# Optimization experiments

Hardware: AMD Instinct MI355X
Metric: run time of the kernel (lower is better)

## Reference

```python
import jax, jax.numpy as jnp
import numpy as np

EPS = 1e-5
K_NBR = 21   # num_neighbors + 1 (self)
PSI = 4


def _bn(x, g, b):
    # BatchNorm (training-mode forward): channel-last, normalize over all other axes
    axes = tuple(range(x.ndim - 1))
    m = jnp.mean(x, axis=axes, keepdims=True)
    v = jnp.var(x, axis=axes, keepdims=True)
    return (x - m) * jax.lax.rsqrt(v + EPS) * g + b


def setup_inputs() -> dict:
    key = jax.random.key(0)
    ks = jax.random.split(key, 16)
    B, N, Cin, Cout = 4, 2048, 64, 256
    h = Cout // 2
    w_ch = Cout // PSI
    heads = 2 * PSI - 1

    def w(k, o, i):
        return jax.random.normal(k, (o, i), dtype=jnp.float32) * (1.0 / np.sqrt(i))

    p = {}
    p['xyz'] = jax.random.normal(ks[0], (B, N, 3), dtype=jnp.float32)
    p['f'] = jax.random.normal(ks[1], (B, Cin, N), dtype=jnp.float32)
    p['W_geo'] = w(ks[2], h, 6);       p['g_geo'] = jnp.ones(h);   p['b_geo'] = jnp.zeros(h)
    p['W_feat'] = w(ks[3], h, 2 * Cin); p['g_feat'] = jnp.ones(h); p['b_feat'] = jnp.zeros(h)
    p['g_bn'] = jnp.ones(Cout); p['b_bn'] = jnp.zeros(Cout)
    p['W_q'] = w(ks[4], Cout, Cout); p['g_q'] = jnp.ones(Cout); p['b_q'] = jnp.zeros(Cout)
    p['W_k'] = w(ks[5], Cout, Cout); p['g_k'] = jnp.ones(Cout); p['b_k'] = jnp.zeros(Cout)
    p['W_v'] = w(ks[6], Cout, Cout); p['g_v'] = jnp.ones(Cout); p['b_v'] = jnp.zeros(Cout)
    p['W_fus'] = w(ks[7], Cout, heads * w_ch); p['bias_fus'] = jnp.zeros(Cout)
    p['g_fus'] = jnp.ones(Cout); p['b_fus'] = jnp.zeros(Cout)
    p['g_ln'] = jnp.ones(Cout); p['b_ln'] = jnp.zeros(Cout)
    p['W_mlp'] = w(ks[8], Cout, Cout); p['bias_mlp'] = jnp.zeros(Cout)
    return p


def reference(xyz, f, W_geo, g_geo, b_geo, W_feat, g_feat, b_feat, g_bn, b_bn,
              W_q, g_q, b_q, W_k, g_k, b_k, W_v, g_v, b_v,
              W_fus, bias_fus, g_fus, b_fus, g_ln, b_ln, W_mlp, bias_mlp):
    B, N, _ = xyz.shape
    Cout = g_bn.shape[0]
    w_ch = Cout // PSI
    d_sh = w_ch // 2
    heads = 2 * PSI - 1

    # ---- PositionFusion: KNN grouping ----
    sq = jnp.sum(xyz * xyz, axis=-1)                                   # [B,N]
    d2 = sq[:, :, None] + sq[:, None, :] - 2.0 * jnp.einsum('bnd,bmd->bnm', xyz, xyz)
    _, idx = jax.lax.top_k(-d2, K_NBR)                                 # [B,N,K]

    grouped_xyz = jax.vmap(lambda p, i: p[i])(xyz, idx)                # [B,N,K,3]
    xyz_diff = grouped_xyz - xyz[:, :, None, :]
    geo_in = jnp.concatenate(
        [jnp.broadcast_to(xyz[:, :, None, :], grouped_xyz.shape), xyz_diff], axis=-1)  # [B,N,K,6]

    ft = jnp.transpose(f, (0, 2, 1))                                   # [B,N,Cin]
    grouped_f = jax.vmap(lambda p, i: p[i])(ft, idx)                   # [B,N,K,Cin]
    feat_in = jnp.concatenate(
        [grouped_f, jnp.broadcast_to(ft[:, :, None, :], grouped_f.shape)], axis=-1)    # [B,N,K,2Cin]

    geo = jax.nn.relu(_bn(jnp.einsum('bnki,oi->bnko', geo_in, W_geo), g_geo, b_geo))
    fea = jax.nn.relu(_bn(jnp.einsum('bnki,oi->bnko', feat_in, W_feat), g_feat, b_feat))
    feature_ = jnp.max(jnp.concatenate([geo, fea], axis=-1), axis=2)   # [B,N,Cout] (maxpool over K)

    # ---- BatchNorm1d ----
    x = _bn(feature_, g_bn, b_bn)

    # ---- Shifted-channel multi-head attention ----
    q = jax.nn.relu(_bn(jnp.einsum('bnc,oc->bno', x, W_q), g_q, b_q))
    k = jax.nn.relu(_bn(jnp.einsum('bnc,oc->bno', x, W_k), g_k, b_k))
    v = jax.nn.relu(_bn(jnp.einsum('bnc,oc->bno', x, W_v), g_v, b_v))

    qh = jnp.stack([q[..., m * d_sh:m * d_sh + w_ch] for m in range(heads)], axis=1)  # [B,H,N,w]
    kh = jnp.stack([k[..., m * d_sh:m * d_sh + w_ch] for m in range(heads)], axis=1)
    vh = jnp.stack([v[..., m * d_sh:m * d_sh + w_ch] for m in range(heads)], axis=1)

    a = jax.nn.softmax(jnp.einsum('bhnc,bhmc->bhnm', qh, kh), axis=-1)  # [B,H,N,N]
    o = jnp.einsum('bhnm,bhmc->bhnc', a, vh)                            # [B,H,N,w]
    O = jnp.transpose(o, (0, 2, 1, 3)).reshape(B, N, heads * w_ch)      # channel-concat per head

    fus = jax.nn.relu(_bn(jnp.einsum('bnc,oc->bno', O, W_fus) + bias_fus, g_fus, b_fus))

    feature__ = fus + feature_                                          # residual

    # ---- LayerNorm over channels ----
    m = jnp.mean(feature__, axis=-1, keepdims=True)
    var = jnp.var(feature__, axis=-1, keepdims=True)
    y = (feature__ - m) * jax.lax.rsqrt(var + EPS) * g_ln + b_ln

    out = feature__ + (jnp.einsum('bnc,oc->bno', y, W_mlp) + bias_mlp)
    return jnp.transpose(out, (0, 2, 1))                                # [B,Cout,N] like torch
```

## Files before the change

### kernel.cpp

```cpp
#include <hip/hip_runtime.h>
#include <math.h>

#define NB    4
#define NPTS  2048
#define ROWS  (NB*NPTS)
#define CIN   64
#define COUT  256
#define KNBR  21
#define NHEADS 7
#define WCH   64
#define DSH   32
#define LOG2E 1.4426950408889634f

typedef __attribute__((ext_vector_type(8))) short short8;
typedef __attribute__((ext_vector_type(4))) float floatx4;

#if __has_builtin(__builtin_amdgcn_exp2f)
#define EXP2(x) __builtin_amdgcn_exp2f(x)
#else
#define EXP2(x) __expf((x)*0.6931471805599453f)
#endif
#if __has_builtin(__builtin_amdgcn_rcpf)
#define RCP(x) __builtin_amdgcn_rcpf(x)
#else
#define RCP(x) (1.0f/(x))
#endif

__device__ __forceinline__ ushort f2bf(float x) {
    unsigned u = __float_as_uint(x);
    u += 0x7fffu + ((u >> 16) & 1u);
    return (ushort)(u >> 16);
}

__device__ __forceinline__ unsigned cvt_pk_bf16(float lo, float hi) {
    unsigned r;
    asm("v_cvt_pk_bf16_f32 %0, %1, %2" : "=v"(r) : "v"(lo), "v"(hi));
    return r;
}

template<int CTRL, int RMASK>
__device__ __forceinline__ unsigned dpp_umin_step(unsigned x) {
    unsigned t = (unsigned)__builtin_amdgcn_update_dpp((int)x, (int)x, CTRL, RMASK, 0xF, false);
    return (t < x) ? t : x;
}
__device__ __forceinline__ unsigned wave_min_u32(unsigned x) {
    x = dpp_umin_step<0x111, 0xF>(x);
    x = dpp_umin_step<0x112, 0xF>(x);
    x = dpp_umin_step<0x114, 0xF>(x);
    x = dpp_umin_step<0x118, 0xF>(x);
    x = dpp_umin_step<0x142, 0xA>(x);
    x = dpp_umin_step<0x143, 0xC>(x);
    return (unsigned)__builtin_amdgcn_readlane((int)x, 63);
}

__device__ __forceinline__ unsigned umin2(unsigned a, unsigned b) { return a < b ? a : b; }
__device__ __forceinline__ unsigned umax2(unsigned a, unsigned b) { return a < b ? b : a; }

__device__ __forceinline__ void ins6(unsigned &m1, unsigned &m2, unsigned &m3,
                                     unsigned &m4, unsigned &m5, unsigned &m6, unsigned k) {
    unsigned c = k, t;
    t = umin2(m1, c); c = umax2(m1, c); m1 = t;
    t = umin2(m2, c); c = umax2(m2, c); m2 = t;
    t = umin2(m3, c); c = umax2(m3, c); m3 = t;
    t = umin2(m4, c); c = umax2(m4, c); m4 = t;
    t = umin2(m5, c); c = umax2(m5, c); m5 = t;
    m6 = umin2(m6, c);
}

__global__ __launch_bounds__(256) void prep_knn(const float* __restrict__ f, const float* __restrict__ Wf,
                                                const float* __restrict__ xyz, const float* __restrict__ Wg,
                                                const float* __restrict__ W_q, const float* __restrict__ W_k,
                                                const float* __restrict__ W_v, const float* __restrict__ W_fus,
                                                float* __restrict__ X, float* __restrict__ A,
                                                ushort* __restrict__ Wb, float* __restrict__ sums,
                                                int* __restrict__ idx) {
    __shared__ float4 SXQ[2048];
    int t = threadIdx.x;
    int blk = blockIdx.x;
    if (blk < 512) {
        float* As = (float*)SXQ;
        float* Ws = As + 16*68;
        int bx = blk & 127, by = blk >> 7;
        if (by == 0 && bx < 12) sums[bx*256 + t] = 0.f;
        int gid = (by*128 + bx)*256 + t;
        for (int i = gid; i < 311296; i += 131072) {
            const float* Wsrc; int off;
            if (i < 65536)       { Wsrc = W_q;   off = i; }
            else if (i < 131072) { Wsrc = W_k;   off = i - 65536; }
            else if (i < 196608) { Wsrc = W_v;   off = i - 131072; }
            else                 { Wsrc = W_fus; off = i - 196608; }
            Wb[i] = f2bf(Wsrc[off]);
        }
        int r0 = bx * 64, n0 = by * 64;
        for (int e = t; e < 4096; e += 256) {
            int row = r0 + (e >> 6), c = n0 + (e & 63), cc = c & 127;
            float x = xyz[row*3], y = xyz[row*3+1], z = xyz[row*3+2];
            const float* w = Wg + cc*6;
            float s = (c < 128) ? ((w[3]*x + w[4]*y) + w[5]*z)
                                : (((w[0]-w[3])*x + (w[1]-w[4])*y) + (w[2]-w[5])*z);
            A[(size_t)row*256 + c] = s;
        }
        int b = r0 >> 11, nbase = r0 & 2047;
        int tx = t & 15, ty = t >> 4;
        float acc[4][4];
#pragma unroll
        for (int i = 0; i < 4; i++)
#pragma unroll
            for (int j = 0; j < 4; j++) acc[i][j] = 0.f;
        int m64 = t & 63, kg = t >> 6;
        int lk = t & 15, lm = t >> 4;
        for (int k0 = 0; k0 < 64; k0 += 16) {
#pragma unroll
            for (int p = 0; p < 4; p++) {
                int k = kg*4 + p;
                As[k*68 + m64] = f[(size_t)b*CIN*NPTS + (size_t)(k0 + k)*NPTS + nbase + m64];
            }
#pragma unroll
            for (int i2 = 0; i2 < 4; i2++) {
                int cg = n0 + lm + 16*i2;
                Ws[lk*68 + lm + 16*i2] = Wf[(size_t)(cg & 127)*128 + (cg >> 7)*64 + k0 + lk];
            }
            __syncthreads();
#pragma unroll
            for (int kq = 0; kq < 16; kq++) {
                float4 a  = *(const float4*)&As[kq*68 + 4*ty];
                float4 b4 = *(const float4*)&Ws[kq*68 + 4*tx];
                float av[4] = {a.x, a.y, a.z, a.w};
                float bv[4] = {b4.x, b4.y, b4.z, b4.w};
#pragma unroll
                for (int i = 0; i < 4; i++)
#pragma unroll
                    for (int j = 0; j < 4; j++) acc[i][j] = fmaf(av[i], bv[j], acc[i][j]);
            }
            __syncthreads();
        }
#pragma unroll
        for (int i = 0; i < 4; i++)
#pragma unroll
            for (int j = 0; j < 4; j++)
                X[(size_t)(r0 + 4*ty + i)*256 + n0 + 4*tx + j] = acc[i][j];
        return;
    }
    int kb = blk - 512;
    int b = kb >> 9;
    int g = kb & 511;
    for (int m = t; m < NPTS; m += 256) {
        float x = xyz[(size_t)b*NPTS*3 + m*3];
        float y = xyz[(size_t)b*NPTS*3 + m*3 + 1];
        float z = xyz[(size_t)b*NPTS*3 + m*3 + 2];
        SXQ[m] = make_float4(x, y, z, (x*x + y*y) + z*z);
    }
    __syncthreads();
    int w = t >> 6, lane = t & 63;
    int n = g*4 + w;
    float4 q4 = SXQ[n];
    float qx = q4.x, qy = q4.y, qz = q4.z, sqn = q4.w;

    unsigned key[32];
    unsigned a1 = 0xFFFFFFFFu, a2 = 0xFFFFFFFFu, a3 = 0xFFFFFFFFu,
             a4 = 0xFFFFFFFFu, a5 = 0xFFFFFFFFu, a6 = 0xFFFFFFFFu;
    unsigned c1 = 0xFFFFFFFFu, c2 = 0xFFFFFFFFu, c3 = 0xFFFFFFFFu,
             c4 = 0xFFFFFFFFu, c5 = 0xFFFFFFFFu, c6 = 0xFFFFFFFFu;
#pragma unroll
    for (int i = 0; i < 16; i++) {
        int m = lane + (i << 6);
        float4 p = SXQ[m];
        float dt = (qx*p.x + qy*p.y) + qz*p.z;
        float d2 = fmaxf((sqn + p.w) - 2.0f*dt, 0.f);
        unsigned kv = (__float_as_uint(d2) & 0xFFFFF800u) | (unsigned)m;
        key[i] = kv;
        ins6(a1, a2, a3, a4, a5, a6, kv);
    }
#pragma unroll
    for (int i = 16; i < 32; i++) {
        int m = lane + (i << 6);
        float4 p = SXQ[m];
        float dt = (qx*p.x + qy*p.y) + qz*p.z;
        float d2 = fmaxf((sqn + p.w) - 2.0f*dt, 0.f);
        unsigned kv = (__float_as_uint(d2) & 0xFFFFF800u) | (unsigned)m;
        key[i] = kv;
        ins6(c1, c2, c3, c4, c5, c6, kv);
    }
    ins6(a1, a2, a3, a4, a5, a6, c1);
    ins6(a1, a2, a3, a4, a5, a6, c2);
    ins6(a1, a2, a3, a4, a5, a6, c3);
    ins6(a1, a2, a3, a4, a5, a6, c4);
    ins6(a1, a2, a3, a4, a5, a6, c5);
    ins6(a1, a2, a3, a4, a5, a6, c6);

    unsigned winkey = 0xFFFFFFFFu;
    {
        unsigned fr = a1, p2 = a2, p3 = a3, p4 = a4, p5 = a5, p6 = a6;
#pragma unroll
        for (int kk = 0; kk < 32; kk++) {
            unsigned win = wave_min_u32(fr);
            if (lane == kk) winkey = win;
            bool own = (fr == win);
            fr = own ? p2 : fr;
            p2 = own ? p3 : p2;
            p3 = own ? p4 : p3;
            p4 = own ? p5 : p4;
            p5 = own ? p6 : p5;
            p6 = own ? 0xFFFFFFFFu : p6;
        }
        if (__ballot(fr == 0xFFFFFFFFu) != 0ULL) {
            winkey = 0xFFFFFFFFu;
            for (int kk = 0; kk < 32; kk++) {
                unsigned lv = key[0];
#pragma unroll
                for (int i = 1; i < 32; i++) lv = (key[i] < lv) ? key[i] : lv;
                unsigned win = wave_min_u32(lv);
                if (lane == kk) winkey = win;
                unsigned widx = win & 2047u;
                int slot = (int)(widx >> 6);
                bool own = (lane == (int)(widx & 63u));
#pragma unroll
                for (int i = 0; i < 32; i++)
                    if (i == slot && own) key[i] = 0xFFFFFFFFu;
            }
        }
    }
    double d2r;
    int mr;
    {
        double qx64 = (double)qx, qy64 = (double)qy, qz64 = (double)qz;
        double sqn64 = qx64*qx64 + qy64*qy64 + qz64*qz64;
        if (lane < 32) {
            mr = (int)(winkey & 2047u);
            float4 p = SXQ[mr];
            double x = (double)p.x, y = (double)p.y, z = (double)p.z;
            double sqm = x*x + y*y + z*z;
            double dt  = qx64*x + qy64*y + qz64*z;
            d2r = (sqn64 + sqm) - 2.0*dt;
        } else {
            d2r = INFINITY; mr = 0x7FFFFFFF;
        }
    }
#pragma unroll
    for (int k = 2; k <= 32; k <<= 1) {
#pragma unroll
        for (int j = k >> 1; j > 0; j >>= 1) {
            double od = __shfl_xor(d2r, j, 64);
            int    om = __shfl_xor(mr, j, 64);
            bool up    = ((lane & k) == 0);
            bool lower = ((lane & j) == 0);
            bool oless = (od < d2r) || (od == d2r && om < mr);
            bool keepOther = up ? (lower ? oless : !oless) : (lower ? !oless : oless);
            if (keepOther) { d2r = od; mr = om; }
        }
    }
    if (lane < KNBR)
        idx[((size_t)b*NPTS + n)*KNBR + lane] = mr;
}

__global__ __launch_bounds__(256) void stats_gf(const float* __restrict__ geoBC, const float* __restrict__ featAC,
                                                const int* __restrict__ idx, const float* __restrict__ g_geo,
                                                const float* __restrict__ g_feat,
                                                float* __restrict__ sums, float* __restrict__ xsel) {
    int c = threadIdx.x;
    int cc = c & 127;
    const float* base = (c < 128) ? geoBC : featAC;
    bool wantmax = ((c < 128) ? g_geo[cc] : g_feat[cc]) >= 0.f;
    float s = 0.f, ss = 0.f;
    int r0 = blockIdx.x * 32;
    for (int r = r0; r < r0 + 32; r++) {
        int b = r >> 11;
        float ctr = base[(size_t)r*256 + 128 + cc];
        float mx = -1e30f, mn = 1e30f;
        const int* ip = idx + (size_t)r*KNBR;
        for (int kk = 0; kk < KNBR; kk++) {
            int j = ip[kk];
            float xv = ctr + base[((size_t)(b*NPTS + j))*256 + cc];
            mx = fmaxf(mx, xv); mn = fminf(mn, xv);
            s += xv; ss += xv*xv;
        }
        xsel[(size_t)r*256 + c] = wantmax ? mx : mn;
    }
    atomicAdd(&sums[c], s);
    atomicAdd(&sums[256 + c], ss);
}

__global__ __launch_bounds__(256) void feature_maxsel(const float* __restrict__ xsel, const float* __restrict__ sums,
                                                      const float* __restrict__ g_geo, const float* __restrict__ b_geo,
                                                      const float* __restrict__ g_feat, const float* __restrict__ b_feat,
                                                      float* __restrict__ feat, float* __restrict__ sums_bn1) {
    int c = threadIdx.x;
    const float inv = 1.0f / (float)(ROWS*KNBR);
    float mean = sums[c]*inv;
    float var  = sums[256+c]*inv - mean*mean;
    float g  = (c < 128) ? g_geo[c] : g_feat[c-128];
    float bb = (c < 128) ? b_geo[c] : b_feat[c-128];
    float sc = g / sqrtf(var + 1e-5f);
    float tt = bb - mean*sc;
    float s = 0.f, ss = 0.f;
    int r0 = blockIdx.x*32;
    for (int r = r0; r < r0+32; r++) {
        size_t i = (size_t)r*256 + c;
        float y = fmaxf(fmaf(sc, xsel[i], tt), 0.f);
        feat[i] = y; s += y; ss += y*y;
    }
    atomicAdd(&sums_bn1[c], s); atomicAdd(&sums_bn1[256+c], ss);
}

__global__ __launch_bounds__(256) void gemm_qkv(const float* __restrict__ Af, const float* __restrict__ sums_in,
                                                const float* __restrict__ g_bn, const float* __restrict__ b_bn,
                                                const ushort* __restrict__ Wb,
                                                float* __restrict__ QKVF, float* __restrict__ sums) {
    __shared__ float bns[2][256];
    __shared__ float red[4][256][2];
    int t = threadIdx.x;
    int r0 = blockIdx.x * 64, g = blockIdx.y;
    int w = t >> 6, lane = t & 63;
    int r15 = lane & 15, quad = lane >> 4;
    {
        float mean = sums_in[512 + t] * (1.0f/(float)ROWS);
        float var  = sums_in[768 + t] * (1.0f/(float)ROWS) - mean*mean;
        float sc = g_bn[t] / sqrtf(var + 1e-5f);
        bns[0][t] = sc;
        bns[1][t] = b_bn[t] - mean*sc;
    }
    __syncthreads();
    short8 aq[8];
    {
        const float* ap = Af + (size_t)(r0 + 16*w + r15)*256;
#pragma unroll
        for (int kc = 0; kc < 8; kc++) {
            int k0 = 32*kc + 8*quad;
            float4 a0 = *(const float4*)&ap[k0];
            float4 a1 = *(const float4*)&ap[k0+4];
            float4 s0 = *(const float4*)&bns[0][k0];
            float4 s1 = *(const float4*)&bns[0][k0+4];
            float4 h0 = *(const float4*)&bns[1][k0];
            float4 h1 = *(const float4*)&bns[1][k0+4];
            ushort u8[8];
            u8[0] = f2bf(fmaf(s0.x, a0.x, h0.x)); u8[1] = f2bf(fmaf(s0.y, a0.y, h0.y));
            u8[2] = f2bf(fmaf(s0.z, a0.z, h0.z)); u8[3] = f2bf(fmaf(s0.w, a0.w, h0.w));
            u8[4] = f2bf(fmaf(s1.x, a1.x, h1.x)); u8[5] = f2bf(fmaf(s1.y, a1.y, h1.y));
            u8[6] = f2bf(fmaf(s1.z, a1.z, h1.z)); u8[7] = f2bf(fmaf(s1.w, a1.w, h1.w));
            aq[kc] = *(short8*)u8;
        }
    }
    floatx4 zero4 = {0.f, 0.f, 0.f, 0.f};
    floatx4 acc[16];
#pragma unroll
    for (int st = 0; st < 16; st++) acc[st] = zero4;
    const ushort* wbase = Wb + (size_t)g*65536 + (size_t)r15*256 + 8*quad;
#pragma unroll
    for (int st = 0; st < 16; st++) {
        const ushort* wp = wbase + (size_t)(16*st)*256;
#pragma unroll
        for (int kc = 0; kc < 8; kc++) {
            short8 bf = *(const short8*)(wp + 32*kc);
            acc[st] = __builtin_amdgcn_mfma_f32_16x16x32_bf16(aq[kc], bf, acc[st], 0, 0, 0);
        }
    }
#pragma unroll
    for (int st = 0; st < 16; st++) {
        float s  = (acc[st][0] + acc[st][1]) + (acc[st][2] + acc[st][3]);
        float q2 = (acc[st][0]*acc[st][0] + acc[st][1]*acc[st][1]) +
                   (acc[st][2]*acc[st][2] + acc[st][3]*acc[st][3]);
        s  += __shfl_xor(s, 16, 64);  s  += __shfl_xor(s, 32, 64);
        q2 += __shfl_xor(q2, 16, 64); q2 += __shfl_xor(q2, 32, 64);
        if (lane < 16) { red[w][16*st + r15][0] = s; red[w][16*st + r15][1] = q2; }
#pragma unroll
        for (int reg = 0; reg < 4; reg++)
            QKVF[(size_t)(r0 + 16*w + 4*quad + reg)*768 + g*256 + 16*st + r15] = acc[st][reg];
    }
    __syncthreads();
    {
        float s = red[0][t][0] + red[1][t][0] + red[2][t][0] + red[3][t][0];
        float q = red[0][t][1] + red[1][t][1] + red[2][t][1] + red[3][t][1];
        atomicAdd(&sums[1024 + g*512 + t], s);
        atomicAdd(&sums[1024 + g*512 + 256 + t], q);
    }
}

__global__ __launch_bounds__(256) void affine_qkv(const float* __restrict__ QKVF, const float* __restrict__ sums,
                                                  const float* __restrict__ g_q, const float* __restrict__ b_q,
                                                  const float* __restrict__ g_k, const float* __restrict__ b_k,
                                                  const float* __restrict__ g_v, const float* __restrict__ b_v,
                                                  ushort* __restrict__ qk, ushort* __restrict__ vt) {
    __shared__ float sts[6][256];
    __shared__ ushort tile[64][72];
    int t = threadIdx.x;
    {
        const float* gs[3] = {g_q, g_k, g_v};
        const float* bs[3] = {b_q, b_k, b_v};
#pragma unroll
        for (int g = 0; g < 3; g++) {
            float mean = sums[1024 + g*512 + t] * (1.0f/(float)ROWS);
            float var  = sums[1024 + g*512 + 256 + t] * (1.0f/(float)ROWS) - mean*mean;
            float sc = gs[g][t] / sqrtf(var + 1e-5f);
            float sh = bs[g][t] - mean*sc;
            if (g == 0) { sc *= LOG2E; sh *= LOG2E; }
            sts[2*g][t] = sc;
            sts[2*g+1][t] = sh;
        }
    }
    __syncthreads();
    int r0 = blockIdx.x * 64, c0 = blockIdx.y * 64;
    int b = r0 >> 11, nbase = r0 & 2047;
    if (c0 < 512) {
#pragma unroll
        for (int rep = 0; rep < 16; rep++) {
            int e = t + 256*rep;
            int row = e >> 6, c = e & 63;
            int col = c0 + c, g = col >> 8, cc = col & 255;
            float v = QKVF[(size_t)(r0 + row)*768 + col];
            v = fmaxf(fmaf(sts[2*g][cc], v, sts[2*g+1][cc]), 0.f);
            qk[(size_t)(r0 + row)*512 + col] = f2bf(v);
        }
    } else {
#pragma unroll
        for (int rep = 0; rep < 16; rep++) {
            int e = t + 256*rep;
            int row = e >> 6, c = e & 63;
            int col = c0 + c, cc = col & 255;
            float v = QKVF[(size_t)(r0 + row)*768 + col];
            v = fmaxf(fmaf(sts[4][cc], v, sts[5][cc]), 0.f);
            tile[c][row] = f2bf(v);
        }
        __syncthreads();
#pragma unroll
        for (int rep = 0; rep < 16; rep++) {
            int e = t + 256*rep;
            int cc = e >> 6, nn = e & 63;
            vt[((size_t)(b*256 + (c0 - 512) + cc))*2048 + nbase + nn] = tile[cc][nn];
        }
    }
}

__global__ __launch_bounds__(512) void attn2(const ushort* __restrict__ qk, const ushort* __restrict__ vt,
                                             float* __restrict__ obuf) {
    __shared__ ushort Ksh[2][64*72];
    __shared__ ushort Vts[2][64*72];
    __shared__ ushort Psh[128*72];
    int h = blockIdx.y, b = blockIdx.z;
    int r0 = blockIdx.x * 128;
    int t = threadIdx.x;
    int w = t >> 6, lane = t & 63;
    int r15 = lane & 15, quad = lane >> 4;
    size_t rowbase = (size_t)b*NPTS;
    int hoff = h*DSH;
    int rr = t >> 3, c8 = t & 7;

    const ushort* ksrc = qk + (rowbase + rr)*512 + 256 + hoff + 8*c8;
    const ushort* vsrc = vt + ((size_t)(b*256 + hoff + rr))*2048 + 8*c8;
    int ldst = rr*72 + 8*c8;

    short8 aq[2];
#pragma unroll
    for (int s = 0; s < 2; s++)
        aq[s] = *(const short8*)(qk + (rowbase + r0 + 16*w + r15)*512 + hoff + 32*s + 8*quad);

    {
        uint4 k0 = *(const uint4*)(ksrc);
        uint4 v0 = *(const uint4*)(vsrc);
        *(uint4*)&Ksh[0][ldst] = k0;
        *(uint4*)&Vts[0][ldst] = v0;
    }

    floatx4 zero4 = {0.f, 0.f, 0.f, 0.f};
    floatx4 oacc[4];
    float mrun = -1e30f, lrun = 0.f;
#pragma unroll
    for (int i = 0; i < 4; i++) oacc[i] = zero4;

    ushort* prow = &Psh[(16*w + r15)*72];

    asm volatile("s_waitcnt lgkmcnt(0)" ::: "memory");
    __builtin_amdgcn_s_barrier();
    __builtin_amdgcn_sched_barrier(0);

    int cur = 0;
    for (int m0 = 0; m0 < NPTS; m0 += 64) {
        int mnext = (m0 + 64 < NPTS) ? (m0 + 64) : 0;
        uint4 kreg = *(const uint4*)(ksrc + (size_t)mnext*512);
        uint4 vreg = *(const uint4*)(vsrc + mnext);

        const ushort* Kc = Ksh[cur];
        const ushort* Vc = Vts[cur];

        floatx4 sacc[4];
#pragma unroll
        for (int tt = 0; tt < 4; tt++) sacc[tt] = zero4;
        __builtin_amdgcn_s_setprio(1);
#pragma unroll
        for (int tt = 0; tt < 4; tt++) {
            int key = 16*tt + r15;
#pragma unroll
            for (int s = 0; s < 2; s++) {
                short8 kf = *(const short8*)&Kc[key*72 + 32*s + 8*quad];
                sacc[tt] = __builtin_amdgcn_mfma_f32_16x16x32_bf16(kf, aq[s], sacc[tt], 0, 0, 0);
            }
        }
        __builtin_amdgcn_s_setprio(0);

        float mx = sacc[0][0];
#pragma unroll
        for (int tt = 0; tt < 4; tt++)
#pragma unroll
            for (int reg = 0; reg < 4; reg++) mx = fmaxf(mx, sacc[tt][reg]);
        mx = fmaxf(mx, __shfl_xor(mx, 16, 64));
        mx = fmaxf(mx, __shfl_xor(mx, 32, 64));

        if (!__all(mx <= mrun)) {
            float mnew = fmaxf(mrun, mx);
            float alpha = EXP2(mrun - mnew);
            lrun *= alpha;
#pragma unroll
            for (int td = 0; td < 4; td++) oacc[td] *= alpha;
            mrun = mnew;
        }

        float rs = 0.f;
#pragma unroll
        for (int tt = 0; tt < 4; tt++) {
            float p0 = EXP2(sacc[tt][0] - mrun);
            float p1 = EXP2(sacc[tt][1] - mrun);
            float p2 = EXP2(sacc[tt][2] - mrun);
            float p3 = EXP2(sacc[tt][3] - mrun);
            rs += (p0 + p1) + (p2 + p3);
            uint2 pk2;
            pk2.x = cvt_pk_bf16(p0, p1);
            pk2.y = cvt_pk_bf16(p2, p3);
            *(uint2*)&prow[16*tt + 4*quad] = pk2;
        }
        rs += __shfl_xor(rs, 16, 64);
        rs += __shfl_xor(rs, 32, 64);
        lrun += rs;

        __builtin_amdgcn_s_setprio(1);
#pragma unroll
        for (int s = 0; s < 2; s++) {
            short8 pf = *(const short8*)&prow[32*s + 8*quad];
#pragma unroll
            for (int td = 0; td < 4; td++) {
                short8 vf = *(const short8*)&Vts[cur][(16*td + r15)*72 + 32*s + 8*quad];
                oacc[td] = __builtin_amdgcn_mfma_f32_16x16x32_bf16(vf, pf, oacc[td], 0, 0, 0);
            }
        }
        __builtin_amdgcn_s_setprio(0);
        (void)Vc;

        *(uint4*)&Ksh[cur ^ 1][ldst] = kreg;
        *(uint4*)&Vts[cur ^ 1][ldst] = vreg;
        cur ^= 1;

        asm volatile("s_waitcnt lgkmcnt(0)" ::: "memory");
        __builtin_amdgcn_s_barrier();
        __builtin_amdgcn_sched_barrier(0);
    }

    float invl = RCP(lrun);
#pragma unroll
    for (int td = 0; td < 4; td++) {
        floatx4 o = oacc[td] * invl;
        *(float4*)&obuf[(rowbase + r0 + 16*w + r15)*(size_t)(NHEADS*WCH) + h*WCH + 16*td + 4*quad] =
            *(float4*)&o;
    }
}

__global__ __launch_bounds__(256) void gemm_fus(const float* __restrict__ OBUF, const ushort* __restrict__ Wb,
                                                const float* __restrict__ bias, float* __restrict__ C,
                                                float* __restrict__ sums) {
    __shared__ float red[4][128][2];
    int t = threadIdx.x;
    int r0 = blockIdx.x * 64, n0 = blockIdx.y * 128;
    int w = t >> 6, lane = t & 63;
    int r15 = lane & 15, quad = lane >> 4;
    int arow = 16*w + r15;
    short8 aq[14];
    {
        const float* p0 = OBUF + (size_t)(r0 + arow)*448;
#pragma unroll
        for (int kc = 0; kc < 14; kc++) {
            int k0 = 32*kc + 8*quad;
            float4 x0 = *(const float4*)&p0[k0];
            float4 y0 = *(const float4*)&p0[k0+4];
            ushort u8[8];
            u8[0] = f2bf(x0.x); u8[1] = f2bf(x0.y);
            u8[2] = f2bf(x0.z); u8[3] = f2bf(x0.w);
            u8[4] = f2bf(y0.x); u8[5] = f2bf(y0.y);
            u8[6] = f2bf(y0.z); u8[7] = f2bf(y0.w);
            aq[kc] = *(short8*)u8;
        }
    }
    floatx4 zero4 = {0.f, 0.f, 0.f, 0.f};
    floatx4 acc[8];
#pragma unroll
    for (int st = 0; st < 8; st++) acc[st] = zero4;
    const ushort* wbase = Wb + 196608 + (size_t)(n0 + r15)*448 + 8*quad;
#pragma unroll
    for (int st = 0; st < 8; st++) {
        const ushort* wp = wbase + (size_t)(16*st)*448;
#pragma unroll
        for (int kc = 0; kc < 14; kc++) {
            short8 bf = *(const short8*)(wp + 32*kc);
            acc[st] = __builtin_amdgcn_mfma_f32_16x16x32_bf16(aq[kc], bf, acc[st], 0, 0, 0);
        }
    }
#pragma unroll
    for (int st = 0; st < 8; st++) {
        int col = n0 + 16*st + r15;
        float bi = bias[col];
        float v0 = acc[st][0] + bi, v1 = acc[st][1] + bi, v2 = acc[st][2] + bi, v3 = acc[st][3] + bi;
        float s  = (v0 + v1) + (v2 + v3);
        float q2 = (v0*v0 + v1*v1) + (v2*v2 + v3*v3);
        s  += __shfl_xor(s, 16, 64);  s  += __shfl_xor(s, 32, 64);
        q2 += __shfl_xor(q2, 16, 64); q2 += __shfl_xor(q2, 32, 64);
        if (lane < 16) { red[w][16*st + r15][0] = s; red[w][16*st + r15][1] = q2; }
        C[(size_t)(r0 + 16*w + 4*quad + 0)*256 + col] = v0;
        C[(size_t)(r0 + 16*w + 4*quad + 1)*256 + col] = v1;
        C[(size_t)(r0 + 16*w + 4*quad + 2)*256 + col] = v2;
        C[(size_t)(r0 + 16*w + 4*quad + 3)*256 + col] = v3;
    }
    __syncthreads();
    {
        int col = t >> 1, which = t & 1;
        float v = red[0][col][which] + red[1][col][which] + red[2][col][which] + red[3][col][which];
        atomicAdd(&sums[2560 + which*256 + n0 + col], v);
    }
}

__global__ __launch_bounds__(256) void gemm_mlp_ln(const float* __restrict__ FUSP, const float* __restrict__ A,
                                                   const float* __restrict__ sums,
                                                   const float* __restrict__ g_fus, const float* __restrict__ b_fus,
                                                   const float* __restrict__ g_ln, const float* __restrict__ b_ln,
                                                   const float* __restrict__ W, const float* __restrict__ bias,
                                                   float* __restrict__ outp) {
    __shared__ float Ys[256][68];
    __shared__ float FFs[64][65];
    __shared__ float Ws[16][68];
    __shared__ float tr[64][65];
    __shared__ float SC[256], SH[256], GL[256], BL[256];
    int t = threadIdx.x;
    int r0 = blockIdx.x*64, n0 = blockIdx.y*64;
    {
        float mean0 = sums[2560 + t] * (1.0f/(float)ROWS);
        float var0  = sums[2560 + 256 + t] * (1.0f/(float)ROWS) - mean0*mean0;
        float sc = g_fus[t] / sqrtf(var0 + 1e-5f);
        SC[t] = sc; SH[t] = b_fus[t] - mean0*sc;
        GL[t] = g_ln[t]; BL[t] = b_ln[t];
    }
    __syncthreads();
    int row = t >> 2, seg = t & 3;
    size_t rb = (size_t)(r0 + row)*256;
    float4 vv[16];
    float s = 0.f, ss = 0.f;
#pragma unroll
    for (int j = 0; j < 16; j++) {
        int c = seg*64 + 4*j;
        float4 fp = *(const float4*)&FUSP[rb + c];
        float4 fe = *(const float4*)&A[rb + c];
        float4 sc4 = *(const float4*)&SC[c];
        float4 sh4 = *(const float4*)&SH[c];
        float4 v;
        v.x = fmaxf(fmaf(sc4.x, fp.x, sh4.x), 0.f) + fe.x;
        v.y = fmaxf(fmaf(sc4.y, fp.y, sh4.y), 0.f) + fe.y;
        v.z = fmaxf(fmaf(sc4.z, fp.z, sh4.z), 0.f) + fe.z;
        v.w = fmaxf(fmaf(sc4.w, fp.w, sh4.w), 0.f) + fe.w;
        vv[j] = v;
        s  += (v.x + v.y) + (v.z + v.w);
        ss += (v.x*v.x + v.y*v.y) + (v.z*v.z + v.w*v.w);
        if (seg == blockIdx.y) *(float4*)&FFs[row][4*j] = v;
    }
    s  += __shfl_xor(s, 1, 64);  s  += __shfl_xor(s, 2, 64);
    ss += __shfl_xor(ss, 1, 64); ss += __shfl_xor(ss, 2, 64);
    float mean = s * (1.f/256.f);
    float var  = ss * (1.f/256.f) - mean*mean;
    float rin  = 1.f/sqrtf(var + 1e-5f);
#pragma unroll
    for (int j = 0; j < 16; j++) {
        int c = seg*64 + 4*j;
        float4 gl = *(const float4*)&GL[c];
        float4 bl = *(const float4*)&BL[c];
        float4 v = vv[j];
        Ys[c+0][row] = (v.x - mean)*rin*gl.x + bl.x;
        Ys[c+1][row] = (v.y - mean)*rin*gl.y + bl.y;
        Ys[c+2][row] = (v.z - mean)*rin*gl.z + bl.z;
        Ys[c+3][row] = (v.w - mean)*rin*gl.w + bl.w;
    }
    __syncthreads();
    int tx = t & 15, ty = t >> 4;
    int lk = t & 15, lm = t >> 4;
    float acc[4][4];
#pragma unroll
    for (int i = 0; i < 4; i++)
#pragma unroll
        for (int j = 0; j < 4; j++) acc[i][j] = 0.f;
    for (int k0 = 0; k0 < 256; k0 += 16) {
#pragma unroll
        for (int i2 = 0; i2 < 4; i2++)
            Ws[lk][lm + 16*i2] = W[(size_t)(n0 + lm + 16*i2)*256 + k0 + lk];
        __syncthreads();
#pragma unroll
        for (int kq = 0; kq < 16; kq++) {
            float4 a  = *(const float4*)&Ys[k0 + kq][4*ty];
            float4 b4 = *(const float4*)&Ws[kq][4*tx];
            float av[4] = {a.x, a.y, a.z, a.w};
            float bv[4] = {b4.x, b4.y, b4.z, b4.w};
#pragma unroll
            for (int i = 0; i < 4; i++)
#pragma unroll
                for (int j = 0; j < 4; j++) acc[i][j] = fmaf(av[i], bv[j], acc[i][j]);
        }
        __syncthreads();
    }
#pragma unroll
    for (int i = 0; i < 4; i++)
#pragma unroll
        for (int j = 0; j < 4; j++) {
            float v = acc[i][j] + bias[n0 + 4*tx + j] + FFs[4*ty + i][4*tx + j];
            tr[4*tx + j][4*ty + i] = v;
        }
    __syncthreads();
    int b = r0 >> 11, nbase = r0 & 2047;
#pragma unroll
    for (int rep = 0; rep < 16; rep++) {
        int e = t + 256*rep;
        int cl = e >> 6, nl = e & 63;
        outp[((size_t)(b*256 + n0 + cl))*2048 + nbase + nl] = tr[cl][nl];
    }
}

extern "C" void kernel_launch(void* const* d_in, const int* in_sizes, int n_in,
                              void* d_out, int out_size, void* d_ws, size_t ws_size,
                              hipStream_t stream) {
    const float* xyz    = (const float*)d_in[0];
    const float* f      = (const float*)d_in[1];
    const float* W_geo  = (const float*)d_in[2];
    const float* g_geo  = (const float*)d_in[3];
    const float* b_geo  = (const float*)d_in[4];
    const float* W_feat = (const float*)d_in[5];
    const float* g_feat = (const float*)d_in[6];
    const float* b_feat = (const float*)d_in[7];
    const float* g_bn   = (const float*)d_in[8];
    const float* b_bn   = (const float*)d_in[9];
    const float* W_q    = (const float*)d_in[10];
    const float* g_q    = (const float*)d_in[11];
    const float* b_q    = (const float*)d_in[12];
    const float* W_k    = (const float*)d_in[13];
    const float* g_k    = (const float*)d_in[14];
    const float* b_k    = (const float*)d_in[15];
    const float* W_v    = (const float*)d_in[16];
    const float* g_v    = (const float*)d_in[17];
    const float* b_v    = (const float*)d_in[18];
    const float* W_fus  = (const float*)d_in[19];
    const float* bias_fus = (const float*)d_in[20];
    const float* g_fus  = (const float*)d_in[21];
    const float* b_fus  = (const float*)d_in[22];
    const float* g_ln   = (const float*)d_in[23];
    const float* b_ln   = (const float*)d_in[24];
    const float* W_mlp  = (const float*)d_in[25];
    const float* bias_mlp = (const float*)d_in[26];

    float* ws = (float*)d_ws;
    const size_t MBF = 262144;
    float* SUMS  = ws;
    int*   IDX   = (int*)(ws + 16384);
    float* A     = ws + 1*MBF;
    float* X     = ws + 9*MBF;
    ushort* QK16 = (ushort*)(ws + 9*MBF);
    float* FUSP  = ws + 9*MBF;
    float* CSEL  = ws + 17*MBF;
    float* QKVF  = ws + 17*MBF;
    float* OBUF  = ws + 17*MBF;
    ushort* VT16 = (ushort*)(ws + 45*MBF);
    ushort* WB16 = (ushort*)(ws + 49*MBF);

    prep_knn<<<2560, 256, 0, stream>>>(f, W_feat, xyz, W_geo, W_q, W_k, W_v, W_fus,
                                       X, A, WB16, SUMS, IDX);
    stats_gf<<<256, 256, 0, stream>>>(A, X, IDX, g_geo, g_feat, SUMS, CSEL);
    feature_maxsel<<<256, 256, 0, stream>>>(CSEL, SUMS, g_geo, b_geo, g_feat, b_feat, A, SUMS + 512);
    gemm_qkv<<<dim3(128, 3), 256, 0, stream>>>(A, SUMS, g_bn, b_bn, WB16, QKVF, SUMS);
    affine_qkv<<<dim3(128, 12), 256, 0, stream>>>(QKVF, SUMS, g_q, b_q, g_k, b_k, g_v, b_v, QK16, VT16);
    attn2<<<dim3(NPTS/128, NHEADS, NB), 512, 0, stream>>>(QK16, VT16, OBUF);
    gemm_fus<<<dim3(128, 2), 256, 0, stream>>>(OBUF, WB16, bias_fus, FUSP, SUMS);
    gemm_mlp_ln<<<dim3(128, 4), 256, 0, stream>>>(FUSP, A, SUMS, g_fus, b_fus, g_ln, b_ln,
                                                  W_mlp, bias_mlp, (float*)d_out);
}
```

Before: 381.8 us.

## Process two query tiles per wave and load V fragments directly from global

The attention kernel now runs 4 waves per block instead of 8, and each wave handles 32 query rows as two 16-row tiles. This lets each K fragment read from shared memory feed two MFMAs. V fragments are no longer staged through shared memory; each wave reads them straight from the transposed V buffer in global memory into registers, and one V fragment is reused across both query tiles. The aim is to cut LDS traffic and barrier work per unit of compute. The cost is more registers per thread and uncoalesced, non-prefetched global V loads issued in the same iteration in which they are used, which may expose latency.

```diff
diff --git a/kernel.cpp b/kernel.cpp
--- a/kernel.cpp
+++ b/kernel.cpp
@@ -430,10 +430,9 @@
     }
 }
 
-__global__ __launch_bounds__(512) void attn2(const ushort* __restrict__ qk, const ushort* __restrict__ vt,
+__global__ __launch_bounds__(256) void attn2(const ushort* __restrict__ qk, const ushort* __restrict__ vt,
                                              float* __restrict__ obuf) {
     __shared__ ushort Ksh[2][64*72];
-    __shared__ ushort Vts[2][64*72];
     __shared__ ushort Psh[128*72];
     int h = blockIdx.y, b = blockIdx.z;
     int r0 = blockIdx.x * 128;
@@ -442,31 +441,39 @@
     int r15 = lane & 15, quad = lane >> 4;
     size_t rowbase = (size_t)b*NPTS;
     int hoff = h*DSH;
-    int rr = t >> 3, c8 = t & 7;
-
-    const ushort* ksrc = qk + (rowbase + rr)*512 + 256 + hoff + 8*c8;
-    const ushort* vsrc = vt + ((size_t)(b*256 + hoff + rr))*2048 + 8*c8;
-    int ldst = rr*72 + 8*c8;
-
-    short8 aq[2];
-#pragma unroll
-    for (int s = 0; s < 2; s++)
-        aq[s] = *(const short8*)(qk + (rowbase + r0 + 16*w + r15)*512 + hoff + 32*s + 8*quad);
+
+    int rr0 = t >> 3, c8 = t & 7;
+    const ushort* ksrc = qk + (rowbase + rr0)*512 + 256 + hoff + 8*c8;
+    int ldst = rr0*72 + 8*c8;
+
+    const ushort* vsrc = vt + ((size_t)(b*256 + hoff + r15))*2048 + 8*quad;
+
+    short8 aq[2][2];
+#pragma unroll
+    for (int u = 0; u < 2; u++)
+#pragma unroll
+        for (int s = 0; s < 2; s++)
+            aq[u][s] = *(const short8*)(qk + (rowbase + r0 + 32*w + 16*u + r15)*512 + hoff + 32*s + 8*quad);
 
     {
         uint4 k0 = *(const uint4*)(ksrc);
-        uint4 v0 = *(const uint4*)(vsrc);
+        uint4 k1 = *(const uint4*)(ksrc + 32*512);
         *(uint4*)&Ksh[0][ldst] = k0;
-        *(uint4*)&Vts[0][ldst] = v0;
+        *(uint4*)&Ksh[0][ldst + 32*72] = k1;
     }
 
     floatx4 zero4 = {0.f, 0.f, 0.f, 0.f};
-    floatx4 oacc[4];
-    float mrun = -1e30f, lrun = 0.f;
-#pragma unroll
-    for (int i = 0; i < 4; i++) oacc[i] = zero4;
-
-    ushort* prow = &Psh[(16*w + r15)*72];
+    floatx4 oacc[2][4];
+    float mrun[2], lrun[2];
+#pragma unroll
+    for (int u = 0; u < 2; u++) {
+        mrun[u] = -1e30f; lrun[u] = 0.f;
+#pragma unroll
+        for (int i = 0; i < 4; i++) oacc[u][i] = zero4;
+    }
+
+    ushort* prow0 = &Psh[(32*w + r15)*72];
+    ushort* prow1 = &Psh[(32*w + 16 + r15)*72];
 
     asm volatile("s_waitcnt lgkmcnt(0)" ::: "memory");
     __builtin_amdgcn_s_barrier();
@@ -475,15 +482,23 @@
     int cur = 0;
     for (int m0 = 0; m0 < NPTS; m0 += 64) {
         int mnext = (m0 + 64 < NPTS) ? (m0 + 64) : 0;
-        uint4 kreg = *(const uint4*)(ksrc + (size_t)mnext*512);
-        uint4 vreg = *(const uint4*)(vsrc + mnext);
+        uint4 kreg0 = *(const uint4*)(ksrc + (size_t)mnext*512);
+        uint4 kreg1 = *(const uint4*)(ksrc + (size_t)mnext*512 + 32*512);
+
+        short8 vreg[2][4];
+#pragma unroll
+        for (int s = 0; s < 2; s++)
+#pragma unroll
+            for (int td = 0; td < 4; td++)
+                vreg[s][td] = *(const short8*)(vsrc + (size_t)(16*td)*2048 + m0 + 32*s);
 
         const ushort* Kc = Ksh[cur];
-        const ushort* Vc = Vts[cur];
-
-        floatx4 sacc[4];
-#pragma unroll
-        for (int tt = 0; tt < 4; tt++) sacc[tt] = zero4;
+
+        floatx4 sacc[2][4];
+#pragma unroll
+        for (int u = 0; u < 2; u++)
+#pragma unroll
+            for (int tt = 0; tt < 4; tt++) sacc[u][tt] = zero4;
         __builtin_amdgcn_s_setprio(1);
 #pragma unroll
         for (int tt = 0; tt < 4; tt++) {
@@ -491,60 +506,66 @@
 #pragma unroll
             for (int s = 0; s < 2; s++) {
                 short8 kf = *(const short8*)&Kc[key*72 + 32*s + 8*quad];
-                sacc[tt] = __builtin_amdgcn_mfma_f32_16x16x32_bf16(kf, aq[s], sacc[tt], 0, 0, 0);
+                sacc[0][tt] = __builtin_amdgcn_mfma_f32_16x16x32_bf16(kf, aq[0][s], sacc[0][tt], 0, 0, 0);
+                sacc[1][tt] = __builtin_amdgcn_mfma_f32_16x16x32_bf16(kf, aq[1][s], sacc[1][tt], 0, 0, 0);
             }
         }
         __builtin_amdgcn_s_setprio(0);
 
-        float mx = sacc[0][0];
-#pragma unroll
-        for (int tt = 0; tt < 4; tt++)
-#pragma unroll
-            for (int reg = 0; reg < 4; reg++) mx = fmaxf(mx, sacc[tt][reg]);
-        mx = fmaxf(mx, __shfl_xor(mx, 16, 64));
-        mx = fmaxf(mx, __shfl_xor(mx, 32, 64));
-
-        if (!__all(mx <= mrun)) {
-            float mnew = fmaxf(mrun, mx);
-            float alpha = EXP2(mrun - mnew);
-            lrun *= alpha;
-#pragma unroll
-            for (int td = 0; td < 4; td++) oacc[td] *= alpha;
-            mrun = mnew;
-        }
-
-        float rs = 0.f;
-#pragma unroll
-        for (int tt = 0; tt < 4; tt++) {
-            float p0 = EXP2(sacc[tt][0] - mrun);
-            float p1 = EXP2(sacc[tt][1] - mrun);
-            float p2 = EXP2(sacc[tt][2] - mrun);
-            float p3 = EXP2(sacc[tt][3] - mrun);
-            rs += (p0 + p1) + (p2 + p3);
-            uint2 pk2;
-            pk2.x = cvt_pk_bf16(p0, p1);
-            pk2.y = cvt_pk_bf16(p2, p3);
-            *(uint2*)&prow[16*tt + 4*quad] = pk2;
-        }
-        rs += __shfl_xor(rs, 16, 64);
-        rs += __shfl_xor(rs, 32, 64);
-        lrun += rs;
+#pragma unroll
+        for (int u = 0; u < 2; u++) {
+            float mx = sacc[u][0][0];
+#pragma unroll
+            for (int tt = 0; tt < 4; tt++)
+#pragma unroll
+                for (int reg = 0; reg < 4; reg++) mx = fmaxf(mx, sacc[u][tt][reg]);
+            mx = fmaxf(mx, __shfl_xor(mx, 16, 64));
+            mx = fmaxf(mx, __shfl_xor(mx, 32, 64));
+
+            if (!__all(mx <= mrun[u])) {
+                float mnew = fmaxf(mrun[u], mx);
+                float alpha = EXP2(mrun[u] - mnew);
+                lrun[u] *= alpha;
+#pragma unroll
+                for (int td = 0; td < 4; td++) oacc[u][td] *= alpha;
+                mrun[u] = mnew;
+            }
+
+            ushort* prow = u ? prow1 : prow0;
+            float rs = 0.f;
+#pragma unroll
+            for (int tt = 0; tt < 4; tt++) {
+                float p0 = EXP2(sacc[u][tt][0] - mrun[u]);
+                float p1 = EXP2(sacc[u][tt][1] - mrun[u]);
+                float p2 = EXP2(sacc[u][tt][2] - mrun[u]);
+                float p3 = EXP2(sacc[u][tt][3] - mrun[u]);
+                rs += (p0 + p1) + (p2 + p3);
+                uint2 pk2;
+                pk2.x = cvt_pk_bf16(p0, p1);
+                pk2.y = cvt_pk_bf16(p2, p3);
+                *(uint2*)&prow[16*tt + 4*quad] = pk2;
+            }
+            rs += __shfl_xor(rs, 16, 64);
+            rs += __shfl_xor(rs, 32, 64);
+            lrun[u] += rs;
+        }
 
         __builtin_amdgcn_s_setprio(1);
 #pragma unroll
         for (int s = 0; s < 2; s++) {
-            short8 pf = *(const short8*)&prow[32*s + 8*quad];
+            short8 pf0 = *(const short8*)&prow0[32*s + 8*quad];
+            short8 pf1 = *(const short8*)&prow1[32*s + 8*quad];
 #pragma unroll
             for (int td = 0; td < 4; td++) {
-                short8 vf = *(const short8*)&Vts[cur][(16*td + r15)*72 + 32*s + 8*quad];
-                oacc[td] = __builtin_amdgcn_mfma_f32_16x16x32_bf16(vf, pf, oacc[td], 0, 0, 0);
+                short8 vf = vreg[s][td];
+                oacc[0][td] = __builtin_amdgcn_mfma_f32_16x16x32_bf16(vf, pf0, oacc[0][td], 0, 0, 0);
+                oacc[1][td] = __builtin_amdgcn_mfma_f32_16x16x32_bf16(vf, pf1, oacc[1][td], 0, 0, 0);
             }
         }
         __builtin_amdgcn_s_setprio(0);
-        (void)Vc;
-
-        *(uint4*)&Ksh[cur ^ 1][ldst] = kreg;
-        *(uint4*)&Vts[cur ^ 1][ldst] = vreg;
+
+        *(uint4*)&Ksh[cur ^ 1][ldst] = kreg0;
+        *(uint4*)&Ksh[cur ^ 1][ldst + 32*72] = kreg1;
         cur ^= 1;
 
         asm volatile("s_waitcnt lgkmcnt(0)" ::: "memory");
@@ -552,12 +573,15 @@
         __builtin_amdgcn_sched_barrier(0);
     }
 
-    float invl = RCP(lrun);
-#pragma unroll
-    for (int td = 0; td < 4; td++) {
-        floatx4 o = oacc[td] * invl;
-        *(float4*)&obuf[(rowbase + r0 + 16*w + r15)*(size_t)(NHEADS*WCH) + h*WCH + 16*td + 4*quad] =
-            *(float4*)&o;
+#pragma unroll
+    for (int u = 0; u < 2; u++) {
+        float invl = RCP(lrun[u]);
+#pragma unroll
+        for (int td = 0; td < 4; td++) {
+            floatx4 o = oacc[u][td] * invl;
+            *(float4*)&obuf[(rowbase + r0 + 32*w + 16*u + r15)*(size_t)(NHEADS*WCH) + h*WCH + 16*td + 4*quad] =
+                *(float4*)&o;
+        }
     }
 }
 
@@ -775,7 +799,7 @@
     feature_maxsel<<<256, 256, 0, stream>>>(CSEL, SUMS, g_geo, b_geo, g_feat, b_feat, A, SUMS + 512);
     gemm_qkv<<<dim3(128, 3), 256, 0, stream>>>(A, SUMS, g_bn, b_bn, WB16, QKVF, SUMS);
     affine_qkv<<<dim3(128, 12), 256, 0, stream>>>(QKVF, SUMS, g_q, b_q, g_k, b_k, g_v, b_v, QK16, VT16);
-    attn2<<<dim3(NPTS/128, NHEADS, NB), 512, 0, stream>>>(QK16, VT16, OBUF);
+    attn2<<<dim3(NPTS/128, NHEADS, NB), 256, 0, stream>>>(QK16, VT16, OBUF);
     gemm_fus<<<dim3(128, 2), 256, 0, stream>>>(OBUF, WB16, bias_fus, FUSP, SUMS);
     gemm_mlp_ln<<<dim3(128, 4), 256, 0, stream>>>(FUSP, A, SUMS, g_fus, b_fus, g_ln, b_ln,
                                                   W_mlp, bias_mlp, (float*)d_out);
```

After: 392.6 us. 1.03x slower.

## Keep softmax probabilities in registers via permuted key order in attention

Applied to the files above, without the earlier changes.

The score MFMA now reads key rows in a permuted order, so each lane's output registers already line up with the B-operand layout of the PV MFMA. The probabilities are packed straight into registers, which removes the per-iteration round trip through the Psh shared buffer. The K/V LDS row stride also changes from 72 to 76 to alter the bank-conflict pattern. This depends on the key permutation matching V's column order exactly, and the new padding may change the LDS alignment of the 16-byte loads.

```diff
diff --git a/kernel.cpp b/kernel.cpp
--- a/kernel.cpp
+++ b/kernel.cpp
@@ -11,6 +11,7 @@
 #define WCH   64
 #define DSH   32
 #define LOG2E 1.4426950408889634f
+#define KLD   76
 
 typedef __attribute__((ext_vector_type(8))) short short8;
 typedef __attribute__((ext_vector_type(4))) float floatx4;
@@ -432,9 +433,8 @@
 
 __global__ __launch_bounds__(512) void attn2(const ushort* __restrict__ qk, const ushort* __restrict__ vt,
                                              float* __restrict__ obuf) {
-    __shared__ ushort Ksh[2][64*72];
-    __shared__ ushort Vts[2][64*72];
-    __shared__ ushort Psh[128*72];
+    __shared__ ushort Ksh[2][64*KLD];
+    __shared__ ushort Vts[2][64*KLD];
     int h = blockIdx.y, b = blockIdx.z;
     int r0 = blockIdx.x * 128;
     int t = threadIdx.x;
@@ -446,7 +446,9 @@
 
     const ushort* ksrc = qk + (rowbase + rr)*512 + 256 + hoff + 8*c8;
     const ushort* vsrc = vt + ((size_t)(b*256 + hoff + rr))*2048 + 8*c8;
-    int ldst = rr*72 + 8*c8;
+    int ldst = rr*KLD + 8*c8;
+
+    int kbase = ((r15 & 12) << 1) + (r15 & 3);
 
     short8 aq[2];
 #pragma unroll
@@ -465,8 +467,6 @@
     float mrun = -1e30f, lrun = 0.f;
 #pragma unroll
     for (int i = 0; i < 4; i++) oacc[i] = zero4;
-
-    ushort* prow = &Psh[(16*w + r15)*72];
 
     asm volatile("s_waitcnt lgkmcnt(0)" ::: "memory");
     __builtin_amdgcn_s_barrier();
@@ -487,10 +487,10 @@
         __builtin_amdgcn_s_setprio(1);
 #pragma unroll
         for (int tt = 0; tt < 4; tt++) {
-            int key = 16*tt + r15;
+            int krow = kbase + ((tt & 1) << 2) + ((tt >> 1) << 5);
 #pragma unroll
             for (int s = 0; s < 2; s++) {
-                short8 kf = *(const short8*)&Kc[key*72 + 32*s + 8*quad];
+                short8 kf = *(const short8*)&Kc[krow*KLD + 32*s + 8*quad];
                 sacc[tt] = __builtin_amdgcn_mfma_f32_16x16x32_bf16(kf, aq[s], sacc[tt], 0, 0, 0);
             }
         }
@@ -513,35 +513,37 @@
             mrun = mnew;
         }
 
+        float pm[4][4];
         float rs = 0.f;
 #pragma unroll
         for (int tt = 0; tt < 4; tt++) {
-            float p0 = EXP2(sacc[tt][0] - mrun);
-            float p1 = EXP2(sacc[tt][1] - mrun);
-            float p2 = EXP2(sacc[tt][2] - mrun);
-            float p3 = EXP2(sacc[tt][3] - mrun);
-            rs += (p0 + p1) + (p2 + p3);
-            uint2 pk2;
-            pk2.x = cvt_pk_bf16(p0, p1);
-            pk2.y = cvt_pk_bf16(p2, p3);
-            *(uint2*)&prow[16*tt + 4*quad] = pk2;
+#pragma unroll
+            for (int reg = 0; reg < 4; reg++) {
+                float p = EXP2(sacc[tt][reg] - mrun);
+                pm[tt][reg] = p; rs += p;
+            }
         }
         rs += __shfl_xor(rs, 16, 64);
         rs += __shfl_xor(rs, 32, 64);
         lrun += rs;
 
+        uint4 pk0, pk1;
+        pk0.x = cvt_pk_bf16(pm[0][0], pm[0][1]); pk0.y = cvt_pk_bf16(pm[0][2], pm[0][3]);
+        pk0.z = cvt_pk_bf16(pm[1][0], pm[1][1]); pk0.w = cvt_pk_bf16(pm[1][2], pm[1][3]);
+        pk1.x = cvt_pk_bf16(pm[2][0], pm[2][1]); pk1.y = cvt_pk_bf16(pm[2][2], pm[2][3]);
+        pk1.z = cvt_pk_bf16(pm[3][0], pm[3][1]); pk1.w = cvt_pk_bf16(pm[3][2], pm[3][3]);
+        short8 pf0 = *(short8*)&pk0;
+        short8 pf1 = *(short8*)&pk1;
+
         __builtin_amdgcn_s_setprio(1);
 #pragma unroll
-        for (int s = 0; s < 2; s++) {
-            short8 pf = *(const short8*)&prow[32*s + 8*quad];
-#pragma unroll
-            for (int td = 0; td < 4; td++) {
-                short8 vf = *(const short8*)&Vts[cur][(16*td + r15)*72 + 32*s + 8*quad];
-                oacc[td] = __builtin_amdgcn_mfma_f32_16x16x32_bf16(vf, pf, oacc[td], 0, 0, 0);
-            }
+        for (int td = 0; td < 4; td++) {
+            short8 vf0 = *(const short8*)&Vc[(16*td + r15)*KLD + 8*quad];
+            oacc[td] = __builtin_amdgcn_mfma_f32_16x16x32_bf16(vf0, pf0, oacc[td], 0, 0, 0);
+            short8 vf1 = *(const short8*)&Vc[(16*td + r15)*KLD + 32 + 8*quad];
+            oacc[td] = __builtin_amdgcn_mfma_f32_16x16x32_bf16(vf1, pf1, oacc[td], 0, 0, 0);
         }
         __builtin_amdgcn_s_setprio(0);
-        (void)Vc;
 
         *(uint4*)&Ksh[cur ^ 1][ldst] = kreg;
         *(uint4*)&Vts[cur ^ 1][ldst] = vreg;
```

Result: slower. 559.4 us (+46.5%).
